# Kernel tuning notes

Hardware: AMD Instinct MI355X
Metric: run time of the kernel (lower is better)

## Reference

```python
import jax, jax.numpy as jnp
import numpy as np

CODEBOOK_SIZE = 8192
DIM = 64
B, N = 4, 4096


def setup_inputs() -> dict:
    key = jax.random.key(0)
    k1, k2 = jax.random.split(key)
    x = jax.random.normal(k1, (B, N, DIM), dtype=jnp.float32)
    node_mask = jnp.ones((B, N), dtype=jnp.float32)
    embed = jax.random.normal(k2, (CODEBOOK_SIZE, DIM), dtype=jnp.float32)
    return {"x": x, "node_mask": node_mask, "embed": embed}


def reference(x, node_mask, embed):
    # x: [B, N, D]; embed: [K, D]; node_mask: [B, N]
    b, n, d = x.shape
    k = embed.shape[0]
    flatten = x.reshape(-1, d)  # [B*N, D]
    dist = -(
        jnp.sum(flatten * flatten, axis=1, keepdims=True)
        - 2.0 * (flatten @ embed.T)
        + jnp.sum(embed * embed, axis=1)[None, :]
    )
    embed_ind = jnp.argmax(dist, axis=-1)  # [B*N] nearest-code assignment
    quantize = embed[embed_ind].reshape(b, n, d)  # codebook gather
    # masked one-hot stats (embed_onehot * node_mask), via segment_sum
    mask_flat = node_mask.reshape(-1)
    counts = jax.ops.segment_sum(mask_flat, embed_ind, num_segments=k)  # [K]
    avg_probs = counts / jnp.asarray(flatten.shape[0], dtype=x.dtype)
    perplexity = jnp.exp(-jnp.sum(avg_probs * jnp.log(avg_probs + 1e-10)))
    return quantize, embed_ind.reshape(b, n), perplexity
```

## Files before the change

### kernel.cpp

```cpp
#include <hip/hip_runtime.h>

typedef __attribute__((ext_vector_type(8))) short short8;
typedef __attribute__((ext_vector_type(4))) float f32x4;

#define ROWS 16384
#define DIM 64
#define NCODES 8192
#define MARGIN 0.008f
#define KT_FB 256
#define CTS_PER_BLOCK 32
#define CCH 2

#define WS_BEST   0
#define WS_COUNTS 131072
#define WS_ENH    163840
#define WS_ESWZ   196608
#define WS_NEED   2293760

__device__ __forceinline__ unsigned long long pack_score(float s, int idx) {
  unsigned u = __float_as_uint(s);
  u ^= (unsigned)((int)u >> 31) | 0x80000000u;
  return ((unsigned long long)u << 32) | (unsigned)(0xFFFF - idx);
}
__device__ __forceinline__ unsigned short bf16hi(float f) {
  unsigned u = __float_as_uint(f);
  return (unsigned short)((u + 0x7FFFu + ((u >> 16) & 1u)) >> 16);
}

__global__ void vq_enorm(const float* __restrict__ embed, float* __restrict__ enh) {
  int k = blockIdx.x * 256 + threadIdx.x;
  const float4* e4 = (const float4*)(embed + (size_t)k * DIM);
  float a = 0.f, b = 0.f, c = 0.f, d = 0.f;
#pragma unroll
  for (int i = 0; i < DIM / 4; ++i) {
    float4 v = e4[i];
    a = fmaf(v.x, v.x, a); b = fmaf(v.y, v.y, b);
    c = fmaf(v.z, v.z, c); d = fmaf(v.w, v.w, d);
  }
  enh[k] = 0.5f * ((a + b) + (c + d));
}

__global__ void vq_prep_e(const float* __restrict__ embed, short* __restrict__ eswz) {
  int u = blockIdx.x * 256 + threadIdx.x;
  int l = u & 63, kc = (u >> 6) & 1, ct = u >> 7;
  int code = ct * 16 + (l & 15);
  int kb = kc * 32 + (l >> 4) * 8;
  const float* er = embed + (size_t)code * DIM + kb;
  short8 h8, l8;
#pragma unroll
  for (int j = 0; j < 8; ++j) {
    float v = er[j];
    unsigned short h = bf16hi(v);
    float r = v - __uint_as_float((unsigned)h << 16);
    h8[j] = (short)h;
    l8[j] = (short)bf16hi(r);
  }
  short8* dst = (short8*)eswz;
  size_t frag = (size_t)ct * 4 + kc * 2;
  dst[(frag + 0) * 64 + l] = h8;
  dst[(frag + 1) * 64 + l] = l8;
}

__global__ __launch_bounds__(256, 8) void vq_screen(
    const float* __restrict__ x, const float* __restrict__ embed,
    const short* __restrict__ eswz, const float* __restrict__ enh,
    unsigned long long* __restrict__ best) {
  const int t = threadIdx.x;
  const int l = t & 63, wid = t >> 6;
  const int cl = l & 15, grp = l >> 4;
  const int row0 = blockIdx.x * 64 + wid * 16;
  const int ct0 = blockIdx.y * CTS_PER_BLOCK;

  __shared__ short8 bstage[2][CCH * 4 * 64];

  const char* gbase = (const char*)eswz + (size_t)ct0 * 4 * 1024;

  {
    char* lb = (char*)&bstage[0][0];
#pragma unroll
    for (int i = 0; i < CCH; ++i) {
      const int e = i * 256 + t;
      __builtin_amdgcn_global_load_lds(
          (const __attribute__((address_space(1))) void*)(gbase + (size_t)e * 16),
          (__attribute__((address_space(3))) void*)(lb + e * 16), 16, 0, 0);
    }
  }

  short8 ahi[2], alo[2];
  {
    const float4* xr4 = (const float4*)(x + (size_t)(row0 + cl) * DIM);
#pragma unroll
    for (int kc = 0; kc < 2; ++kc) {
      const int q = kc * 8 + grp * 2;
      float4 v0 = xr4[q], v1 = xr4[q + 1];
      float vv[8] = {v0.x, v0.y, v0.z, v0.w, v1.x, v1.y, v1.z, v1.w};
#pragma unroll
      for (int j = 0; j < 8; ++j) {
        unsigned short h = bf16hi(vv[j]);
        float r = vv[j] - __uint_as_float((unsigned)h << 16);
        ahi[kc][j] = (short)h;
        alo[kc][j] = (short)bf16hi(r);
      }
    }
  }

  float bsc[4];
  int bidx[4];
#pragma unroll
  for (int j = 0; j < 4; ++j) { bsc[j] = -3.4e38f; bidx[j] = 0; }

  __syncthreads();

  for (int ch = 0; ch < CTS_PER_BLOCK / CCH; ++ch) {
    const int cur = ch & 1;
    if (ch + 1 < CTS_PER_BLOCK / CCH) {
      const char* gb = gbase + (size_t)(ch + 1) * CCH * 4 * 1024;
      char* lb = (char*)&bstage[cur ^ 1][0];
#pragma unroll
      for (int i = 0; i < CCH; ++i) {
        const int e = i * 256 + t;
        __builtin_amdgcn_global_load_lds(
            (const __attribute__((address_space(1))) void*)(gb + (size_t)e * 16),
            (__attribute__((address_space(3))) void*)(lb + e * 16), 16, 0, 0);
      }
    }

    const short8* bs = &bstage[cur][0];
#pragma unroll
    for (int cil = 0; cil < CCH; ++cil) {
      const int ci = ch * CCH + cil;
      const float eh = enh[(ct0 + ci) * 16 + cl];
      short8 h0 = bs[(cil * 4 + 0) * 64 + l], l0 = bs[(cil * 4 + 1) * 64 + l];
      short8 h1 = bs[(cil * 4 + 2) * 64 + l], l1 = bs[(cil * 4 + 3) * 64 + l];

      f32x4 acc = {-eh, -eh, -eh, -eh};
      acc = __builtin_amdgcn_mfma_f32_16x16x32_bf16(ahi[0], h0, acc, 0, 0, 0);
      acc = __builtin_amdgcn_mfma_f32_16x16x32_bf16(alo[0], h0, acc, 0, 0, 0);
      acc = __builtin_amdgcn_mfma_f32_16x16x32_bf16(ahi[0], l0, acc, 0, 0, 0);
      acc = __builtin_amdgcn_mfma_f32_16x16x32_bf16(ahi[1], h1, acc, 0, 0, 0);
      acc = __builtin_amdgcn_mfma_f32_16x16x32_bf16(alo[1], h1, acc, 0, 0, 0);
      acc = __builtin_amdgcn_mfma_f32_16x16x32_bf16(ahi[1], l1, acc, 0, 0, 0);

      const int code = (ct0 + ci) * 16 + cl;
#pragma unroll
      for (int j = 0; j < 4; ++j) {
        if (acc[j] > bsc[j]) { bsc[j] = acc[j]; bidx[j] = code; }
      }
    }
    __syncthreads();
  }

  unsigned fmask = 0;
#pragma unroll
  for (int j = 0; j < 4; ++j) {
    float m = bsc[j];
    m = fmaxf(m, __shfl_xor(m, 1));
    m = fmaxf(m, __shfl_xor(m, 2));
    m = fmaxf(m, __shfl_xor(m, 4));
    m = fmaxf(m, __shfl_xor(m, 8));
    if (bsc[j] >= m - MARGIN) fmask |= 1u << j;
  }

  float exact[4];
#pragma unroll
  for (int j = 0; j < 4; ++j) exact[j] = -3.4e38f;

  while (__any((int)(fmask != 0))) {
    const bool act = fmask != 0;
    const int sel = act ? __ffs(fmask) - 1 : 0;
    int code = 0;
#pragma unroll
    for (int j = 0; j < 4; ++j) code = (sel == j) ? bidx[j] : code;
    int row = act ? (row0 + grp * 4 + sel) : row0;
    if (!act) code = 0;
    const float4* xr = (const float4*)(x + (size_t)row * DIM);
    const float4* er = (const float4*)(embed + (size_t)code * DIM);
    float a0 = 0, a1 = 0, a2 = 0, a3 = 0, n0 = 0, n1 = 0, n2 = 0, n3 = 0;
#pragma unroll
    for (int i = 0; i < 16; ++i) {
      float4 xv = xr[i], ev = er[i];
      a0 = fmaf(xv.x, ev.x, a0); a1 = fmaf(xv.y, ev.y, a1);
      a2 = fmaf(xv.z, ev.z, a2); a3 = fmaf(xv.w, ev.w, a3);
      n0 = fmaf(ev.x, ev.x, n0); n1 = fmaf(ev.y, ev.y, n1);
      n2 = fmaf(ev.z, ev.z, n2); n3 = fmaf(ev.w, ev.w, n3);
    }
    float ex = ((a0 + a1) + (a2 + a3)) - 0.5f * ((n0 + n1) + (n2 + n3));
#pragma unroll
    for (int j = 0; j < 4; ++j)
      exact[j] = (act && sel == j) ? ex : exact[j];
    fmask = act ? (fmask & (fmask - 1)) : 0u;
  }

#pragma unroll
  for (int j = 0; j < 4; ++j) {
    unsigned long long pk = pack_score(exact[j], bidx[j]);
    unsigned long long o;
    o = __shfl_xor(pk, 1); pk = pk > o ? pk : o;
    o = __shfl_xor(pk, 2); pk = pk > o ? pk : o;
    o = __shfl_xor(pk, 4); pk = pk > o ? pk : o;
    o = __shfl_xor(pk, 8); pk = pk > o ? pk : o;
    if (cl == 0) atomicMax(&best[row0 + grp * 4 + j], pk);
  }
}

__global__ __launch_bounds__(256, 2) void vq_score_fb(
    const float* __restrict__ x, const float* __restrict__ embed,
    const float* __restrict__ enh, unsigned long long* __restrict__ best) {
  const int row = blockIdx.x * 256 + threadIdx.x;
  const int c0 = blockIdx.y * KT_FB;
  float4 xa[16];
  const float4* xg = (const float4*)(x + (size_t)row * DIM);
#pragma unroll
  for (int i = 0; i < 16; ++i) xa[i] = xg[i];
  float bs = -3.4e38f;
  int bc = 0;
#pragma unroll 2
  for (int c = c0; c < c0 + KT_FB; ++c) {
    const float4* e4 = (const float4*)(embed + (size_t)c * DIM);
    float a0 = 0.f, a1 = 0.f, a2 = 0.f, a3 = 0.f;
#pragma unroll
    for (int i = 0; i < 16; ++i) {
      float4 ev = e4[i];
      a0 = fmaf(xa[i].x, ev.x, a0); a1 = fmaf(xa[i].y, ev.y, a1);
      a2 = fmaf(xa[i].z, ev.z, a2); a3 = fmaf(xa[i].w, ev.w, a3);
    }
    float s = ((a0 + a1) + (a2 + a3)) - enh[c];
    if (s > bs) { bs = s; bc = c; }
  }
  atomicMax(&best[row], pack_score(bs, bc));
}

__global__ void vq_finalize(const unsigned long long* __restrict__ best,
                            const float* __restrict__ embed,
                            const float* __restrict__ node_mask,
                            float* __restrict__ quant,
                            float* __restrict__ out_idx,
                            float* __restrict__ counts) {
  int gid = blockIdx.x * 256 + threadIdx.x;
  int row = gid >> 6, d = gid & 63;
  unsigned long long p = best[row];
  int idx = 0xFFFF - (int)(p & 0xFFFFull);
  quant[gid] = embed[(size_t)idx * DIM + d];
  if (d == 0) {
    out_idx[row] = (float)idx;
    atomicAdd(&counts[idx], node_mask[row]);
  }
}

__global__ void vq_perplexity(const float* __restrict__ counts, float* __restrict__ out) {
  int tid = threadIdx.x;
  float acc = 0.f;
  for (int k = tid; k < NCODES; k += 256) {
    float p = counts[k] * (1.0f / (float)ROWS);
    acc += p * logf(p + 1e-10f);
  }
#pragma unroll
  for (int off = 32; off > 0; off >>= 1) acc += __shfl_down(acc, off);
  __shared__ float red[4];
  if ((tid & 63) == 0) red[tid >> 6] = acc;
  __syncthreads();
  if (tid == 0) out[0] = expf(-((red[0] + red[1]) + (red[2] + red[3])));
}

extern "C" void kernel_launch(void* const* d_in, const int* in_sizes, int n_in,
                              void* d_out, int out_size, void* d_ws, size_t ws_size,
                              hipStream_t stream) {
  const float* x = (const float*)d_in[0];
  const float* node_mask = (const float*)d_in[1];
  const float* embed = (const float*)d_in[2];

  float* out = (float*)d_out;
  float* quant = out;
  float* out_idx = out + (size_t)ROWS * DIM;
  float* out_ppl = out_idx + ROWS;

  unsigned long long* best = (unsigned long long*)((char*)d_ws + WS_BEST);
  float* counts = (float*)((char*)d_ws + WS_COUNTS);
  float* enh = (float*)((char*)d_ws + WS_ENH);
  short* eswz = (short*)((char*)d_ws + WS_ESWZ);

  hipMemsetAsync(d_ws, 0, WS_ENH, stream);
  vq_enorm<<<NCODES / 256, 256, 0, stream>>>(embed, enh);
  if (ws_size >= WS_NEED) {
    vq_prep_e<<<256, 256, 0, stream>>>(embed, eswz);
    vq_screen<<<dim3(ROWS / 64, NCODES / (CTS_PER_BLOCK * 16)), 256, 0, stream>>>(
        x, embed, eswz, enh, best);
  } else {
    vq_score_fb<<<dim3(ROWS / 256, NCODES / KT_FB), 256, 0, stream>>>(x, embed, enh, best);
  }
  vq_finalize<<<ROWS * DIM / 256, 256, 0, stream>>>(best, embed, node_mask, quant, out_idx, counts);
  vq_perplexity<<<1, 256, 0, stream>>>(counts, out_ppl);
}
```

Baseline: 118.9 us.

## Switch screening GEMM to 32x32x16 MFMA tiles with direct global B loads

Rewrites the screening kernel to use 32x32x16 bf16 MFMA: each wave handles 32 rows against 32-code tiles, and the codebook fragments are re-swizzled to match that layout. The LDS double-buffered staging with per-chunk barriers is removed; B fragments are read straight from global memory or cache. The aim is higher MFMA efficiency per instruction and less synchronisation overhead. In exchange, register pressure rises from 16 accumulators plus per-row best arrays, occupancy drops (launch bounds lowered to 4), and every wave now re-reads codebook data from global memory.

```diff
diff --git a/kernel.cpp b/kernel.cpp
--- a/kernel.cpp
+++ b/kernel.cpp
@@ -2,14 +2,14 @@
 
 typedef __attribute__((ext_vector_type(8))) short short8;
 typedef __attribute__((ext_vector_type(4))) float f32x4;
+typedef __attribute__((ext_vector_type(16))) float f32x16;
 
 #define ROWS 16384
 #define DIM 64
 #define NCODES 8192
 #define MARGIN 0.008f
 #define KT_FB 256
-#define CTS_PER_BLOCK 32
-#define CCH 2
+#define TILES_PER_BLOCK 16
 
 #define WS_BEST   0
 #define WS_COUNTS 131072
@@ -42,9 +42,10 @@
 
 __global__ void vq_prep_e(const float* __restrict__ embed, short* __restrict__ eswz) {
   int u = blockIdx.x * 256 + threadIdx.x;
-  int l = u & 63, kc = (u >> 6) & 1, ct = u >> 7;
-  int code = ct * 16 + (l & 15);
-  int kb = kc * 32 + (l >> 4) * 8;
+  int l = u & 63, fi = (u >> 6) & 7, tile = u >> 9;
+  int term = fi >> 2, kc = fi & 3;
+  int code = tile * 32 + (l & 31);
+  int kb = kc * 16 + (l >> 5) * 8;
   const float* er = embed + (size_t)code * DIM + kb;
   short8 h8, l8;
 #pragma unroll
@@ -55,44 +56,28 @@
     h8[j] = (short)h;
     l8[j] = (short)bf16hi(r);
   }
-  short8* dst = (short8*)eswz;
-  size_t frag = (size_t)ct * 4 + kc * 2;
-  dst[(frag + 0) * 64 + l] = h8;
-  dst[(frag + 1) * 64 + l] = l8;
-}
-
-__global__ __launch_bounds__(256, 8) void vq_screen(
+  ((short8*)eswz)[u] = term ? l8 : h8;
+}
+
+#define MFMA32(A, B, C) __builtin_amdgcn_mfma_f32_32x32x16_bf16((A), (B), (C), 0, 0, 0)
+
+__global__ __launch_bounds__(256, 4) void vq_screen(
     const float* __restrict__ x, const float* __restrict__ embed,
     const short* __restrict__ eswz, const float* __restrict__ enh,
     unsigned long long* __restrict__ best) {
   const int t = threadIdx.x;
   const int l = t & 63, wid = t >> 6;
-  const int cl = l & 15, grp = l >> 4;
-  const int row0 = blockIdx.x * 64 + wid * 16;
-  const int ct0 = blockIdx.y * CTS_PER_BLOCK;
-
-  __shared__ short8 bstage[2][CCH * 4 * 64];
-
-  const char* gbase = (const char*)eswz + (size_t)ct0 * 4 * 1024;
-
+  const int c32 = l & 31, half = l >> 5;
+  const int row0 = blockIdx.x * 128 + wid * 32;
+  const int ty0 = blockIdx.y * TILES_PER_BLOCK;
+
+  short8 ahi[4], alo[4];
   {
-    char* lb = (char*)&bstage[0][0];
-#pragma unroll
-    for (int i = 0; i < CCH; ++i) {
-      const int e = i * 256 + t;
-      __builtin_amdgcn_global_load_lds(
-          (const __attribute__((address_space(1))) void*)(gbase + (size_t)e * 16),
-          (__attribute__((address_space(3))) void*)(lb + e * 16), 16, 0, 0);
-    }
-  }
-
-  short8 ahi[2], alo[2];
-  {
-    const float4* xr4 = (const float4*)(x + (size_t)(row0 + cl) * DIM);
-#pragma unroll
-    for (int kc = 0; kc < 2; ++kc) {
-      const int q = kc * 8 + grp * 2;
-      float4 v0 = xr4[q], v1 = xr4[q + 1];
+    const float* xr = x + (size_t)(row0 + c32) * DIM;
+#pragma unroll
+    for (int kc = 0; kc < 4; ++kc) {
+      const float4* p = (const float4*)(xr + kc * 16 + half * 8);
+      float4 v0 = p[0], v1 = p[1];
       float vv[8] = {v0.x, v0.y, v0.z, v0.w, v1.x, v1.y, v1.z, v1.w};
 #pragma unroll
       for (int j = 0; j < 8; ++j) {
@@ -104,75 +89,72 @@
     }
   }
 
-  float bsc[4];
-  int bidx[4];
-#pragma unroll
-  for (int j = 0; j < 4; ++j) { bsc[j] = -3.4e38f; bidx[j] = 0; }
-
-  __syncthreads();
-
-  for (int ch = 0; ch < CTS_PER_BLOCK / CCH; ++ch) {
-    const int cur = ch & 1;
-    if (ch + 1 < CTS_PER_BLOCK / CCH) {
-      const char* gb = gbase + (size_t)(ch + 1) * CCH * 4 * 1024;
-      char* lb = (char*)&bstage[cur ^ 1][0];
-#pragma unroll
-      for (int i = 0; i < CCH; ++i) {
-        const int e = i * 256 + t;
-        __builtin_amdgcn_global_load_lds(
-            (const __attribute__((address_space(1))) void*)(gb + (size_t)e * 16),
-            (__attribute__((address_space(3))) void*)(lb + e * 16), 16, 0, 0);
-      }
-    }
-
-    const short8* bs = &bstage[cur][0];
-#pragma unroll
-    for (int cil = 0; cil < CCH; ++cil) {
-      const int ci = ch * CCH + cil;
-      const float eh = enh[(ct0 + ci) * 16 + cl];
-      short8 h0 = bs[(cil * 4 + 0) * 64 + l], l0 = bs[(cil * 4 + 1) * 64 + l];
-      short8 h1 = bs[(cil * 4 + 2) * 64 + l], l1 = bs[(cil * 4 + 3) * 64 + l];
-
-      f32x4 acc = {-eh, -eh, -eh, -eh};
-      acc = __builtin_amdgcn_mfma_f32_16x16x32_bf16(ahi[0], h0, acc, 0, 0, 0);
-      acc = __builtin_amdgcn_mfma_f32_16x16x32_bf16(alo[0], h0, acc, 0, 0, 0);
-      acc = __builtin_amdgcn_mfma_f32_16x16x32_bf16(ahi[0], l0, acc, 0, 0, 0);
-      acc = __builtin_amdgcn_mfma_f32_16x16x32_bf16(ahi[1], h1, acc, 0, 0, 0);
-      acc = __builtin_amdgcn_mfma_f32_16x16x32_bf16(alo[1], h1, acc, 0, 0, 0);
-      acc = __builtin_amdgcn_mfma_f32_16x16x32_bf16(ahi[1], l1, acc, 0, 0, 0);
-
-      const int code = (ct0 + ci) * 16 + cl;
-#pragma unroll
-      for (int j = 0; j < 4; ++j) {
-        if (acc[j] > bsc[j]) { bsc[j] = acc[j]; bidx[j] = code; }
-      }
-    }
-    __syncthreads();
+  float bsc[16];
+  int bidx[16];
+#pragma unroll
+  for (int r = 0; r < 16; ++r) { bsc[r] = -3.4e38f; bidx[r] = 0; }
+
+  const short8* eb = (const short8*)eswz + (size_t)ty0 * 8 * 64;
+
+#pragma unroll 2
+  for (int ct = 0; ct < TILES_PER_BLOCK; ++ct) {
+    const short8* bt = eb + (size_t)ct * 512;
+    const float eh = enh[(ty0 + ct) * 32 + c32];
+
+    short8 bh0 = bt[0 * 64 + l], bh1 = bt[1 * 64 + l];
+    short8 bh2 = bt[2 * 64 + l], bh3 = bt[3 * 64 + l];
+
+    f32x16 acc;
+#pragma unroll
+    for (int r = 0; r < 16; ++r) acc[r] = 0.f;
+
+    acc = MFMA32(ahi[0], bh0, acc);
+    acc = MFMA32(ahi[1], bh1, acc);
+    acc = MFMA32(ahi[2], bh2, acc);
+    acc = MFMA32(ahi[3], bh3, acc);
+    acc = MFMA32(alo[0], bh0, acc);
+    acc = MFMA32(alo[1], bh1, acc);
+    acc = MFMA32(alo[2], bh2, acc);
+    acc = MFMA32(alo[3], bh3, acc);
+
+    short8 bl0 = bt[4 * 64 + l], bl1 = bt[5 * 64 + l];
+    short8 bl2 = bt[6 * 64 + l], bl3 = bt[7 * 64 + l];
+    acc = MFMA32(ahi[0], bl0, acc);
+    acc = MFMA32(ahi[1], bl1, acc);
+    acc = MFMA32(ahi[2], bl2, acc);
+    acc = MFMA32(ahi[3], bl3, acc);
+
+#pragma unroll
+    for (int r = 0; r < 16; ++r) {
+      float s = acc[r] - eh;
+      if (s > bsc[r]) { bsc[r] = s; bidx[r] = ct; }
+    }
   }
 
   unsigned fmask = 0;
 #pragma unroll
-  for (int j = 0; j < 4; ++j) {
-    float m = bsc[j];
+  for (int r = 0; r < 16; ++r) {
+    float m = bsc[r];
     m = fmaxf(m, __shfl_xor(m, 1));
     m = fmaxf(m, __shfl_xor(m, 2));
     m = fmaxf(m, __shfl_xor(m, 4));
     m = fmaxf(m, __shfl_xor(m, 8));
-    if (bsc[j] >= m - MARGIN) fmask |= 1u << j;
-  }
-
-  float exact[4];
-#pragma unroll
-  for (int j = 0; j < 4; ++j) exact[j] = -3.4e38f;
+    m = fmaxf(m, __shfl_xor(m, 16));
+    if (bsc[r] >= m - MARGIN) fmask |= 1u << r;
+  }
+
+  float exact[16];
+#pragma unroll
+  for (int r = 0; r < 16; ++r) exact[r] = -3.4e38f;
 
   while (__any((int)(fmask != 0))) {
     const bool act = fmask != 0;
     const int sel = act ? __ffs(fmask) - 1 : 0;
-    int code = 0;
-#pragma unroll
-    for (int j = 0; j < 4; ++j) code = (sel == j) ? bidx[j] : code;
-    int row = act ? (row0 + grp * 4 + sel) : row0;
-    if (!act) code = 0;
+    int ctl = 0;
+#pragma unroll
+    for (int r = 0; r < 16; ++r) ctl = (sel == r) ? bidx[r] : ctl;
+    int code = act ? (ty0 + ctl) * 32 + c32 : 0;
+    int row = act ? row0 + (sel & 3) + 8 * (sel >> 2) + 4 * half : row0;
     const float4* xr = (const float4*)(x + (size_t)row * DIM);
     const float4* er = (const float4*)(embed + (size_t)code * DIM);
     float a0 = 0, a1 = 0, a2 = 0, a3 = 0, n0 = 0, n1 = 0, n2 = 0, n3 = 0;
@@ -186,20 +168,22 @@
     }
     float ex = ((a0 + a1) + (a2 + a3)) - 0.5f * ((n0 + n1) + (n2 + n3));
 #pragma unroll
-    for (int j = 0; j < 4; ++j)
-      exact[j] = (act && sel == j) ? ex : exact[j];
+    for (int r = 0; r < 16; ++r)
+      exact[r] = (act && sel == r) ? ex : exact[r];
     fmask = act ? (fmask & (fmask - 1)) : 0u;
   }
 
 #pragma unroll
-  for (int j = 0; j < 4; ++j) {
-    unsigned long long pk = pack_score(exact[j], bidx[j]);
+  for (int r = 0; r < 16; ++r) {
+    unsigned long long pk = pack_score(exact[r], (ty0 + bidx[r]) * 32 + c32);
     unsigned long long o;
     o = __shfl_xor(pk, 1); pk = pk > o ? pk : o;
     o = __shfl_xor(pk, 2); pk = pk > o ? pk : o;
     o = __shfl_xor(pk, 4); pk = pk > o ? pk : o;
     o = __shfl_xor(pk, 8); pk = pk > o ? pk : o;
-    if (cl == 0) atomicMax(&best[row0 + grp * 4 + j], pk);
+    o = __shfl_xor(pk, 16); pk = pk > o ? pk : o;
+    if (c32 == 0)
+      atomicMax(&best[row0 + (r & 3) + 8 * (r >> 2) + 4 * half], pk);
   }
 }
 
@@ -282,8 +266,8 @@
   hipMemsetAsync(d_ws, 0, WS_ENH, stream);
   vq_enorm<<<NCODES / 256, 256, 0, stream>>>(embed, enh);
   if (ws_size >= WS_NEED) {
-    vq_prep_e<<<256, 256, 0, stream>>>(embed, eswz);
-    vq_screen<<<dim3(ROWS / 64, NCODES / (CTS_PER_BLOCK * 16)), 256, 0, stream>>>(
+    vq_prep_e<<<512, 256, 0, stream>>>(embed, eswz);
+    vq_screen<<<dim3(ROWS / 128, NCODES / (TILES_PER_BLOCK * 32)), 256, 0, stream>>>(
         x, embed, eswz, enh, best);
   } else {
     vq_score_fb<<<dim3(ROWS / 256, NCODES / KT_FB), 256, 0, stream>>>(x, embed, enh, best);
```

Result: slower. 135.7 us (+14.1%).
